# Optimization experiments

Hardware: AMD Instinct MI355X
Metric: run time of the kernel (lower is better)

## Reference

```python
import jax, jax.numpy as jnp
import numpy as np

N_NODES = 20000
N_EDGES = 240000
IN_DIM = 20
SH_DIM = 16  # (lmax+1)^2 with lmax=3
DENOM = 1.0
EPS = 1e-12


def spherical_harmonics_lmax3(v):
    """Real spherical harmonics l=0..3 on unit vectors v: [E,3] -> [E,16]."""
    x, y, z = v[:, 0], v[:, 1], v[:, 2]
    x2, y2, z2 = x * x, y * y, z * z
    sh = [
        jnp.full_like(x, 0.28209479177387814),            # l=0
        0.4886025119029199 * y,                            # l=1, m=-1
        0.4886025119029199 * z,                            # l=1, m=0
        0.4886025119029199 * x,                            # l=1, m=1
        1.0925484305920792 * x * y,                        # l=2, m=-2
        1.0925484305920792 * y * z,                        # l=2, m=-1
        0.31539156525252005 * (3.0 * z2 - 1.0),            # l=2, m=0
        1.0925484305920792 * x * z,                        # l=2, m=1
        0.5462742152960396 * (x2 - y2),                    # l=2, m=2
        0.5900435899266435 * y * (3.0 * x2 - y2),          # l=3, m=-3
        2.890611442640554 * x * y * z,                     # l=3, m=-2
        0.4570457994644658 * y * (5.0 * z2 - 1.0),         # l=3, m=-1
        0.3731763325901154 * z * (5.0 * z2 - 3.0),         # l=3, m=0
        0.4570457994644658 * x * (5.0 * z2 - 1.0),         # l=3, m=1
        1.445305721320277 * z * (x2 - y2),                 # l=3, m=2
        0.5900435899266435 * x * (x2 - 3.0 * y2),          # l=3, m=3
    ]
    return jnp.stack(sh, axis=-1)


def setup_inputs() -> dict:
    key = jax.random.key(0)
    ks = jax.random.split(key, 10)
    x = jax.random.normal(ks[0], (N_NODES, IN_DIM), dtype=jnp.float32)
    positions = jax.random.normal(ks[1], (N_NODES, 3), dtype=jnp.float32)
    edge_index = jax.random.randint(ks[2], (2, N_EDGES), 0, N_NODES, dtype=jnp.int32)
    s = 1.0 / np.sqrt(IN_DIM)
    W_pre = jax.random.uniform(ks[3], (IN_DIM, IN_DIM), jnp.float32, -s, s)
    b_pre = jax.random.uniform(ks[4], (IN_DIM,), jnp.float32, -s, s)
    W_post = jax.random.uniform(ks[5], (IN_DIM, IN_DIM), jnp.float32, -s, s)
    b_post = jax.random.uniform(ks[6], (IN_DIM,), jnp.float32, -s, s)
    W_sc = jax.random.uniform(ks[7], (IN_DIM, IN_DIM), jnp.float32, -s, s)
    b_sc = jax.random.uniform(ks[8], (IN_DIM,), jnp.float32, -s, s)
    return {"x": x, "positions": positions, "edge_index": edge_index,
            "W_pre": W_pre, "b_pre": b_pre, "W_post": W_post, "b_post": b_post,
            "W_sc": W_sc, "b_sc": b_sc}


def reference(x, positions, edge_index, W_pre, b_pre, W_post, b_post, W_sc, b_sc):
    row, col = edge_index[0], edge_index[1]
    # per-edge gather + relative positions
    rel = positions[col] - positions[row]                      # [E,3]
    norm = jnp.sqrt(jnp.sum(rel * rel, axis=-1, keepdims=True) + EPS)
    sh = spherical_harmonics_lmax3(rel / norm)                 # [E,16]
    sender = x[row]                                            # [E,20]
    # equivariant tensor product (outer product over irreps channels)
    tp = (sender[:, :, None] * sh[:, None, :]).reshape(sender.shape[0], IN_DIM * SH_DIM)  # [E,320]
    edge_features = jnp.concatenate([sender, tp], axis=1)      # [E,340]
    # scatter-add aggregation to target nodes
    aggr = jax.ops.segment_sum(edge_features, col, num_segments=N_NODES)  # [N,340]
    # node update MLP + shortcut (math of Layer.update)
    h = x / DENOM
    h = jax.nn.relu(h @ W_pre.T + b_pre)
    h = h @ W_post.T + b_post
    out = x @ W_sc.T + b_sc + h                                # [N,20]
    # aggr is computed (and aggregated) by the original propagate; concat so it stays live
    return jnp.concatenate([out, aggr], axis=1)                # [N,360]
```

## Files before the change

### kernel.cpp

```cpp
#include <hip/hip_runtime.h>

#define N_NODES 20000
#define N_EDGES 240000
#define IN_DIM  20
#define AGG_DIM 340
#define OUT_DIM 360
#define EPS_F   1e-12f
#define CAP     64
#define EDGE_BLOCKS ((N_EDGES + 255) / 256)
#define MLP_BLOCKS  ((N_NODES + 255) / 256)

__device__ __forceinline__ float sh_coeff(int k, float xn, float yn, float zn) {
    const float x2 = xn * xn, y2 = yn * yn, z2 = zn * zn;
    switch (k) {
        case 0:  return 0.28209479177387814f;
        case 1:  return 0.4886025119029199f * yn;
        case 2:  return 0.4886025119029199f * zn;
        case 3:  return 0.4886025119029199f * xn;
        case 4:  return 1.0925484305920792f * xn * yn;
        case 5:  return 1.0925484305920792f * yn * zn;
        case 6:  return 0.31539156525252005f * (3.0f * z2 - 1.0f);
        case 7:  return 1.0925484305920792f * xn * zn;
        case 8:  return 0.5462742152960396f * (x2 - y2);
        case 9:  return 0.5900435899266435f * yn * (3.0f * x2 - y2);
        case 10: return 2.890611442640554f  * xn * yn * zn;
        case 11: return 0.4570457994644658f * yn * (5.0f * z2 - 1.0f);
        case 12: return 0.3731763325901154f * zn * (5.0f * z2 - 3.0f);
        case 13: return 0.4570457994644658f * xn * (5.0f * z2 - 1.0f);
        case 14: return 1.445305721320277f  * zn * (x2 - y2);
        default: return 0.5900435899266435f * xn * (x2 - 3.0f * y2);
    }
}

__global__ __launch_bounds__(256) void bucket_sh_mlp(
    const float* __restrict__ pos,
    const int* __restrict__ ei,
    const float* __restrict__ x,
    const float* __restrict__ Wpre,  const float* __restrict__ bpre,
    const float* __restrict__ Wpost, const float* __restrict__ bpost,
    const float* __restrict__ Wsc,   const float* __restrict__ bsc,
    int* __restrict__ counts,
    int* __restrict__ ovf_cnt,
    int* __restrict__ ovf,
    int* __restrict__ bucket,
    float4* __restrict__ shbuf,
    float* __restrict__ out)
{
    if ((int)blockIdx.x < EDGE_BLOCKS) {
        const int e = (int)(blockIdx.x * 256 + threadIdx.x);
        if (e >= N_EDGES) return;
        const int row = ei[e];
        const int col = ei[N_EDGES + e];
        const int slot = atomicAdd(&counts[col], 1);
        if (slot >= CAP) { ovf[atomicAdd(ovf_cnt, 1)] = e; return; }

        const int sidx = col * CAP + slot;
        bucket[sidx] = row;

        const float rx = pos[col * 3 + 0] - pos[row * 3 + 0];
        const float ry = pos[col * 3 + 1] - pos[row * 3 + 1];
        const float rz = pos[col * 3 + 2] - pos[row * 3 + 2];
        const float rinv = rsqrtf(rx * rx + ry * ry + rz * rz + EPS_F);
        const float xx = rx * rinv, yy = ry * rinv, zz = rz * rinv;
        const float x2 = xx * xx, y2 = yy * yy, z2 = zz * zz;

        const float sh0  = 0.28209479177387814f;
        const float sh1  = 0.4886025119029199f * yy;
        const float sh2  = 0.4886025119029199f * zz;
        const float sh3  = 0.4886025119029199f * xx;
        const float sh4  = 1.0925484305920792f * xx * yy;
        const float sh5  = 1.0925484305920792f * yy * zz;
        const float sh6  = 0.31539156525252005f * (3.0f * z2 - 1.0f);
        const float sh7  = 1.0925484305920792f * xx * zz;
        const float sh8  = 0.5462742152960396f * (x2 - y2);
        const float sh9  = 0.5900435899266435f * yy * (3.0f * x2 - y2);
        const float sh10 = 2.890611442640554f  * xx * yy * zz;
        const float sh11 = 0.4570457994644658f * yy * (5.0f * z2 - 1.0f);
        const float sh12 = 0.3731763325901154f * zz * (5.0f * z2 - 3.0f);
        const float sh13 = 0.4570457994644658f * xx * (5.0f * z2 - 1.0f);
        const float sh14 = 1.445305721320277f  * zz * (x2 - y2);
        const float sh15 = 0.5900435899266435f * xx * (x2 - 3.0f * y2);

        float4* dst = shbuf + (size_t)sidx * 4;
        dst[0] = make_float4(sh12, sh13, sh14, sh15);
        dst[1] = make_float4(sh0,  sh1,  sh2,  sh3);
        dst[2] = make_float4(sh4,  sh5,  sh6,  sh7);
        dst[3] = make_float4(sh8,  sh9,  sh10, sh11);
        return;
    }

    __shared__ float sWpre[IN_DIM * IN_DIM];
    __shared__ float sWpost[IN_DIM * IN_DIM];
    __shared__ float sWsc[IN_DIM * IN_DIM];
    __shared__ float sb[3 * IN_DIM];

    for (int t = threadIdx.x; t < IN_DIM * IN_DIM; t += 256) {
        sWpre[t]  = Wpre[t];
        sWpost[t] = Wpost[t];
        sWsc[t]   = Wsc[t];
    }
    if (threadIdx.x < IN_DIM) {
        sb[threadIdx.x]              = bpre[threadIdx.x];
        sb[IN_DIM + threadIdx.x]     = bpost[threadIdx.x];
        sb[2 * IN_DIM + threadIdx.x] = bsc[threadIdx.x];
    }
    __syncthreads();

    const int i = (int)((blockIdx.x - EDGE_BLOCKS) * 256 + threadIdx.x);
    if (i >= N_NODES) return;

    float xi[IN_DIM], h[IN_DIM];
#pragma unroll
    for (int j = 0; j < IN_DIM; ++j) xi[j] = x[(size_t)i * IN_DIM + j];

#pragma unroll
    for (int j = 0; j < IN_DIM; ++j) {
        float a = sb[j];
#pragma unroll
        for (int kk = 0; kk < IN_DIM; ++kk) a = fmaf(xi[kk], sWpre[j * IN_DIM + kk], a);
        h[j] = fmaxf(a, 0.0f);
    }
#pragma unroll
    for (int j = 0; j < IN_DIM; ++j) {
        float a = sb[IN_DIM + j] + sb[2 * IN_DIM + j];
#pragma unroll
        for (int kk = 0; kk < IN_DIM; ++kk) {
            a = fmaf(h[kk],  sWpost[j * IN_DIM + kk], a);
            a = fmaf(xi[kk], sWsc[j * IN_DIM + kk],  a);
        }
        out[(size_t)i * OUT_DIM + j] = a;
    }
}

__global__ __launch_bounds__(256) void node_gather(
    const float* __restrict__ x,
    const float* __restrict__ pos,
    const int* __restrict__ ei,
    const int* __restrict__ counts,
    const int* __restrict__ bucket,
    const float* __restrict__ shbuf,
    const int* __restrict__ ovf_cnt,
    const int* __restrict__ ovf,
    float* __restrict__ out)
{
    const int lane   = threadIdx.x & 63;
    const int node   = (int)((blockIdx.x * blockDim.x + threadIdx.x) >> 6);
    const int lane20 = min(lane, IN_DIM - 1);
    const int lane16 = lane & 15;

    const int j0 = (lane >= IN_DIM) ? ((lane - IN_DIM) >> 4) : 0;
    const int j1 = (lane + 44)  >> 4;
    const int j2 = (lane + 108) >> 4;
    const int j3 = (lane + 172) >> 4;
    const int j4 = (lane + 236) >> 4;
    const int j5 = (lane + 300) >> 4;

    const int cnt_raw = __builtin_amdgcn_readfirstlane(counts[node]);
    const int cnt = min(cnt_raw, CAP);

    float acc0 = 0.f, acc1 = 0.f, acc2 = 0.f, acc3 = 0.f, acc4 = 0.f, acc5 = 0.f;
    float sum_s = 0.f;

    if (cnt > 0) {
        const int rl = bucket[node * CAP + min(lane, cnt - 1)];
        const float* shb = shbuf + (size_t)node * CAP * 16 + lane16;

        for (int base = 0; base < cnt; base += 4) {
            const int i1 = min(base + 1, cnt - 1);
            const int i2 = min(base + 2, cnt - 1);
            const int i3 = min(base + 3, cnt - 1);
            const int r0 = __builtin_amdgcn_readlane(rl, base);
            const int r1 = __builtin_amdgcn_readlane(rl, i1);
            const int r2 = __builtin_amdgcn_readlane(rl, i2);
            const int r3 = __builtin_amdgcn_readlane(rl, i3);

            float sA = x[(size_t)r0 * IN_DIM + lane20];
            float sB = x[(size_t)r1 * IN_DIM + lane20];
            float sC = x[(size_t)r2 * IN_DIM + lane20];
            float sD = x[(size_t)r3 * IN_DIM + lane20];
            const float shA = shb[(size_t)base * 16];
            const float shB = shb[(size_t)i1 * 16];
            const float shC = shb[(size_t)i2 * 16];
            const float shD = shb[(size_t)i3 * 16];

            sB = (base + 1 < cnt) ? sB : 0.0f;
            sC = (base + 2 < cnt) ? sC : 0.0f;
            sD = (base + 3 < cnt) ? sD : 0.0f;

#define ACCUM(S, SH)                                      \
            sum_s += (S);                                 \
            acc0 = fmaf(__shfl((S), j0, 64), (SH), acc0); \
            acc1 = fmaf(__shfl((S), j1, 64), (SH), acc1); \
            acc2 = fmaf(__shfl((S), j2, 64), (SH), acc2); \
            acc3 = fmaf(__shfl((S), j3, 64), (SH), acc3); \
            acc4 = fmaf(__shfl((S), j4, 64), (SH), acc4); \
            acc5 = fmaf(__shfl((S), j5, 64), (SH), acc5);

            ACCUM(sA, shA)
            ACCUM(sB, shB)
            ACCUM(sC, shC)
            ACCUM(sD, shD)
        }
    }

    if (cnt_raw > CAP) {
        const int m = *ovf_cnt;
        const int k = (lane + 12) & 15;
        for (int i = 0; i < m; ++i) {
            const int e = ovf[i];
            if (ei[N_EDGES + e] != node) continue;
            const int row = ei[e];
            const float rx = pos[node * 3 + 0] - pos[row * 3 + 0];
            const float ry = pos[node * 3 + 1] - pos[row * 3 + 1];
            const float rz = pos[node * 3 + 2] - pos[row * 3 + 2];
            const float rinv = rsqrtf(rx * rx + ry * ry + rz * rz + EPS_F);
            const float shk = sh_coeff(k, rx * rinv, ry * rinv, rz * rinv);
            const float s = x[(size_t)row * IN_DIM + lane20];
            ACCUM(s, shk)
        }
    }
#undef ACCUM

    float* obase = out + (size_t)node * OUT_DIM + IN_DIM;
    obase[lane]       = (lane < IN_DIM) ? sum_s : acc0;
    obase[lane + 64]  = acc1;
    obase[lane + 128] = acc2;
    obase[lane + 192] = acc3;
    obase[lane + 256] = acc4;
    if (lane < IN_DIM) obase[lane + 320] = acc5;
}

extern "C" void kernel_launch(void* const* d_in, const int* in_sizes, int n_in,
                              void* d_out, int out_size, void* d_ws, size_t ws_size,
                              hipStream_t stream)
{
    const float* x     = (const float*)d_in[0];
    const float* pos   = (const float*)d_in[1];
    const int*   ei    = (const int*)d_in[2];
    const float* Wpre  = (const float*)d_in[3];
    const float* bpre  = (const float*)d_in[4];
    const float* Wpost = (const float*)d_in[5];
    const float* bpost = (const float*)d_in[6];
    const float* Wsc   = (const float*)d_in[7];
    const float* bsc   = (const float*)d_in[8];
    float* out = (float*)d_out;

    float4* shbuf = (float4*)d_ws;
    int* ws_i    = (int*)(shbuf + (size_t)N_NODES * CAP * 4);
    int* counts  = ws_i;
    int* ovf_cnt = ws_i + N_NODES;
    int* ovf     = ws_i + N_NODES + 1;
    int* bucket  = ws_i + N_NODES + 1 + N_EDGES;

    hipMemsetAsync(counts, 0, (size_t)(N_NODES + 1) * sizeof(int), stream);

    bucket_sh_mlp<<<EDGE_BLOCKS + MLP_BLOCKS, 256, 0, stream>>>(
        pos, ei, x, Wpre, bpre, Wpost, bpost, Wsc, bsc,
        counts, ovf_cnt, ovf, bucket, shbuf, out);

    node_gather<<<(N_NODES * 64) / 256, 256, 0, stream>>>(
        x, pos, ei, counts, bucket, (const float*)shbuf, ovf_cnt, ovf, out);
}
```

Baseline: 127.5 us.

## Store spherical harmonics in fp16 and software-pipeline gather loads

New measurement: 126.7 us. No clear change (-0.6%).

```diff
diff --git a/kernel.cpp b/kernel.cpp
--- a/kernel.cpp
+++ b/kernel.cpp
@@ -9,6 +9,8 @@
 #define CAP     64
 #define EDGE_BLOCKS ((N_EDGES + 255) / 256)
 #define MLP_BLOCKS  ((N_NODES + 255) / 256)
+
+typedef _Float16 half8 __attribute__((ext_vector_type(8)));
 
 __device__ __forceinline__ float sh_coeff(int k, float xn, float yn, float zn) {
     const float x2 = xn * xn, y2 = yn * yn, z2 = zn * zn;
@@ -43,7 +45,7 @@
     int* __restrict__ ovf_cnt,
     int* __restrict__ ovf,
     int* __restrict__ bucket,
-    float4* __restrict__ shbuf,
+    half8* __restrict__ shbuf,
     float* __restrict__ out)
 {
     if ((int)blockIdx.x < EDGE_BLOCKS) {
@@ -81,11 +83,13 @@
         const float sh14 = 1.445305721320277f  * zz * (x2 - y2);
         const float sh15 = 0.5900435899266435f * xx * (x2 - 3.0f * y2);
 
-        float4* dst = shbuf + (size_t)sidx * 4;
-        dst[0] = make_float4(sh12, sh13, sh14, sh15);
-        dst[1] = make_float4(sh0,  sh1,  sh2,  sh3);
-        dst[2] = make_float4(sh4,  sh5,  sh6,  sh7);
-        dst[3] = make_float4(sh8,  sh9,  sh10, sh11);
+        const half8 v0 = { (_Float16)sh12, (_Float16)sh13, (_Float16)sh14, (_Float16)sh15,
+                           (_Float16)sh0,  (_Float16)sh1,  (_Float16)sh2,  (_Float16)sh3 };
+        const half8 v1 = { (_Float16)sh4,  (_Float16)sh5,  (_Float16)sh6,  (_Float16)sh7,
+                           (_Float16)sh8,  (_Float16)sh9,  (_Float16)sh10, (_Float16)sh11 };
+        half8* dst = shbuf + (size_t)sidx * 2;
+        dst[0] = v0;
+        dst[1] = v1;
         return;
     }
 
@@ -138,7 +142,7 @@
     const int* __restrict__ ei,
     const int* __restrict__ counts,
     const int* __restrict__ bucket,
-    const float* __restrict__ shbuf,
+    const _Float16* __restrict__ shbuf,
     const int* __restrict__ ovf_cnt,
     const int* __restrict__ ovf,
     float* __restrict__ out)
@@ -161,46 +165,66 @@
     float acc0 = 0.f, acc1 = 0.f, acc2 = 0.f, acc3 = 0.f, acc4 = 0.f, acc5 = 0.f;
     float sum_s = 0.f;
 
+#define ACCUM(S, SH)                                      \
+    do {                                                  \
+        sum_s += (S);                                     \
+        acc0 = fmaf(__shfl((S), j0, 64), (SH), acc0);     \
+        acc1 = fmaf(__shfl((S), j1, 64), (SH), acc1);     \
+        acc2 = fmaf(__shfl((S), j2, 64), (SH), acc2);     \
+        acc3 = fmaf(__shfl((S), j3, 64), (SH), acc3);     \
+        acc4 = fmaf(__shfl((S), j4, 64), (SH), acc4);     \
+        acc5 = fmaf(__shfl((S), j5, 64), (SH), acc5);     \
+    } while (0)
+
     if (cnt > 0) {
         const int rl = bucket[node * CAP + min(lane, cnt - 1)];
-        const float* shb = shbuf + (size_t)node * CAP * 16 + lane16;
+        const _Float16* shb = shbuf + (size_t)node * CAP * 16 + lane16;
+
+#define LOADCHUNK(B, S0, S1, S2, S3, H0, H1, H2, H3)                      \
+    do {                                                                  \
+        const int q1 = min((B) + 1, cnt - 1);                             \
+        const int q2 = min((B) + 2, cnt - 1);                             \
+        const int q3 = min((B) + 3, cnt - 1);                             \
+        const int r0 = __builtin_amdgcn_readlane(rl, (B));                \
+        const int r1 = __builtin_amdgcn_readlane(rl, q1);                 \
+        const int r2 = __builtin_amdgcn_readlane(rl, q2);                 \
+        const int r3 = __builtin_amdgcn_readlane(rl, q3);                 \
+        S0 = x[(size_t)r0 * IN_DIM + lane20];                             \
+        S1 = x[(size_t)r1 * IN_DIM + lane20];                             \
+        S2 = x[(size_t)r2 * IN_DIM + lane20];                             \
+        S3 = x[(size_t)r3 * IN_DIM + lane20];                             \
+        H0 = (float)shb[(size_t)(B) * 16];                                \
+        H1 = (float)shb[(size_t)q1 * 16];                                 \
+        H2 = (float)shb[(size_t)q2 * 16];                                 \
+        H3 = (float)shb[(size_t)q3 * 16];                                 \
+    } while (0)
+
+        float sA, sB, sC, sD, shA, shB, shC, shD;
+        float tA, tB, tC, tD, uA, uB, uC, uD;
+
+        LOADCHUNK(0, sA, sB, sC, sD, shA, shB, shC, shD);
 
         for (int base = 0; base < cnt; base += 4) {
-            const int i1 = min(base + 1, cnt - 1);
-            const int i2 = min(base + 2, cnt - 1);
-            const int i3 = min(base + 3, cnt - 1);
-            const int r0 = __builtin_amdgcn_readlane(rl, base);
-            const int r1 = __builtin_amdgcn_readlane(rl, i1);
-            const int r2 = __builtin_amdgcn_readlane(rl, i2);
-            const int r3 = __builtin_amdgcn_readlane(rl, i3);
-
-            float sA = x[(size_t)r0 * IN_DIM + lane20];
-            float sB = x[(size_t)r1 * IN_DIM + lane20];
-            float sC = x[(size_t)r2 * IN_DIM + lane20];
-            float sD = x[(size_t)r3 * IN_DIM + lane20];
-            const float shA = shb[(size_t)base * 16];
-            const float shB = shb[(size_t)i1 * 16];
-            const float shC = shb[(size_t)i2 * 16];
-            const float shD = shb[(size_t)i3 * 16];
-
-            sB = (base + 1 < cnt) ? sB : 0.0f;
-            sC = (base + 2 < cnt) ? sC : 0.0f;
-            sD = (base + 3 < cnt) ? sD : 0.0f;
-
-#define ACCUM(S, SH)                                      \
-            sum_s += (S);                                 \
-            acc0 = fmaf(__shfl((S), j0, 64), (SH), acc0); \
-            acc1 = fmaf(__shfl((S), j1, 64), (SH), acc1); \
-            acc2 = fmaf(__shfl((S), j2, 64), (SH), acc2); \
-            acc3 = fmaf(__shfl((S), j3, 64), (SH), acc3); \
-            acc4 = fmaf(__shfl((S), j4, 64), (SH), acc4); \
-            acc5 = fmaf(__shfl((S), j5, 64), (SH), acc5);
-
-            ACCUM(sA, shA)
-            ACCUM(sB, shB)
-            ACCUM(sC, shC)
-            ACCUM(sD, shD)
+            const int nb = base + 4;
+            const bool have_next = nb < cnt;
+            if (have_next)
+                LOADCHUNK(nb, tA, tB, tC, tD, uA, uB, uC, uD);
+
+            const float mB = (base + 1 < cnt) ? sB : 0.0f;
+            const float mC = (base + 2 < cnt) ? sC : 0.0f;
+            const float mD = (base + 3 < cnt) ? sD : 0.0f;
+
+            ACCUM(sA, shA);
+            ACCUM(mB, shB);
+            ACCUM(mC, shC);
+            ACCUM(mD, shD);
+
+            if (have_next) {
+                sA = tA; sB = tB; sC = tC; sD = tD;
+                shA = uA; shB = uB; shC = uC; shD = uD;
+            }
         }
+#undef LOADCHUNK
     }
 
     if (cnt_raw > CAP) {
@@ -216,7 +240,7 @@
             const float rinv = rsqrtf(rx * rx + ry * ry + rz * rz + EPS_F);
             const float shk = sh_coeff(k, rx * rinv, ry * rinv, rz * rinv);
             const float s = x[(size_t)row * IN_DIM + lane20];
-            ACCUM(s, shk)
+            ACCUM(s, shk);
         }
     }
 #undef ACCUM
@@ -245,8 +269,8 @@
     const float* bsc   = (const float*)d_in[8];
     float* out = (float*)d_out;
 
-    float4* shbuf = (float4*)d_ws;
-    int* ws_i    = (int*)(shbuf + (size_t)N_NODES * CAP * 4);
+    half8* shbuf = (half8*)d_ws;
+    int* ws_i    = (int*)((char*)d_ws + (size_t)N_NODES * CAP * 16 * sizeof(_Float16));
     int* counts  = ws_i;
     int* ovf_cnt = ws_i + N_NODES;
     int* ovf     = ws_i + N_NODES + 1;
@@ -259,5 +283,5 @@
         counts, ovf_cnt, ovf, bucket, shbuf, out);
 
     node_gather<<<(N_NODES * 64) / 256, 256, 0, stream>>>(
-        x, pos, ei, counts, bucket, (const float*)shbuf, ovf_cnt, ovf, out);
-}
+        x, pos, ei, counts, bucket, (const _Float16*)shbuf, ovf_cnt, ovf, out);
+}
```
